# Performance work log

Measured on AMD Instinct MI355X. Metric: run time of the kernel, lower is better.

## Reference

```python
import jax, jax.numpy as jnp
import numpy as np

N_TOKENS = 16384
MODEL_DIM = 2048
NUM_EXPERTS = 16
TOP_K = 2
CAPACITY_FACTOR = 1.0
NUM_SPLIT = 2  # os.environ 'num_split' default in source


def setup_inputs() -> dict:
    key = jax.random.key(0)
    kx, kw = jax.random.split(key)
    x = jax.random.normal(kx, (N_TOKENS, MODEL_DIM), dtype=jnp.float32)
    # kaiming_normal_ on Linear weight: std = sqrt(2 / fan_in)
    wg = jax.random.normal(kw, (NUM_EXPERTS, MODEL_DIM), dtype=jnp.float32) * np.float32(np.sqrt(2.0 / MODEL_DIM))
    return {"x": x, "wg": wg}


def _loss_compute(logits):
    gates = jax.nn.softmax(logits, axis=1)              # [N, E]
    num_experts = logits.shape[1]
    indices1_s = jnp.argmax(gates, axis=1)              # [N]
    mask1 = jax.nn.one_hot(indices1_s, num_experts, dtype=gates.dtype)
    me = jnp.mean(gates, axis=0)
    ce = jnp.mean(mask1, axis=0)
    l_aux = jnp.sum(me * ce) * num_experts
    return l_aux, indices1_s, gates


def _dispatch_fix_capacity(gates, k, capacity_factor, num_split):
    # gates is detached in the original (torch .detach())
    gates = jax.lax.stop_gradient(gates)
    n, e = gates.shape
    capacity = int(k * n // e * capacity_factor) // num_split * num_split
    values, topk_idx = jax.lax.top_k(gates, k)          # [N, k]
    weights = values
    flat_experts = topk_idx.reshape(-1)                 # [N*k]
    order = jnp.argsort(flat_experts)                   # stable sort by expert id
    experts_sorted = flat_experts[order]
    token_ids = jnp.repeat(jnp.arange(n, dtype=jnp.int32), k)[order]
    # position of each routed token within its expert's run
    counts = jax.ops.segment_sum(jnp.ones_like(flat_experts, dtype=jnp.int32), flat_experts, num_segments=e)
    starts = jnp.cumsum(counts) - counts                # exclusive prefix sum
    pos = jnp.arange(n * k, dtype=jnp.int32) - starts[experts_sorted]
    # fixed-capacity index table, -1 = empty slot; overflow tokens dropped
    ind = jnp.full((e, capacity), -1, dtype=jnp.int32)
    ind = ind.at[experts_sorted, pos].set(token_ids, mode="drop")  # pos>=capacity dropped
    indices = ind.reshape(-1)                           # [E*capacity], expert-major
    mask = indices >= 0
    expert_ids = jnp.repeat(jnp.arange(e, dtype=gates.dtype), capacity)
    return weights, indices, expert_ids, mask


def reference(x, wg):
    logits = jnp.einsum("nd,ed->ne", x, wg)             # Linear, no bias
    l_aux, _indices1, gates = _loss_compute(logits)
    weights, indices, expert_ids, mask = _dispatch_fix_capacity(
        gates, TOP_K, CAPACITY_FACTOR, NUM_SPLIT)
    return l_aux, weights, indices, expert_ids
```

## Files before the change

kernel.cpp:

```cpp
#include <hip/hip_runtime.h>
#include <hip/hip_bf16.h>
#include <stdint.h>

#define N_TOKENS    16384
#define MODEL_DIM   2048
#define NUM_EXPERTS 16
#define CAPACITY    2048
#define NBLK2       512
#define NBLK        256
#define GBLK        512
#define W_OFF       1
#define IDX_OFF     (1 + 2 * N_TOKENS)
#define EID_OFF     (IDX_OFF + NUM_EXPERTS * CAPACITY)

#define SC_E01    0
#define SC_CNTH   16384
#define SC_CEH    32768
#define SC_ME     49152

#define DPPX(v, ctrl) __int_as_float(__builtin_amdgcn_update_dpp(             \
    0, __float_as_int(v), (ctrl), 0xF, 0xF, true))
#define SWZ(v, off) __int_as_float(__builtin_amdgcn_ds_swizzle(               \
    __float_as_int(v), (off)))

__global__ __launch_bounds__(512) void k_logits(
    const float* __restrict__ x, const float* __restrict__ wg,
    float* __restrict__ out, uint8_t* __restrict__ ws)
{
  __shared__ float part[8][32][2][17];
  const int tid = threadIdx.x;
  const int b = blockIdx.x;
  const int l = tid & 63;
  const int kr = tid >> 6;
  const int kb = kr * 256 + l * 4;
  const int rot = l & 15;

  float4 w[16];
#pragma unroll
  for (int i = 0; i < NUM_EXPERTS; ++i)
    w[i] = *reinterpret_cast<const float4*>(wg + (size_t)((i ^ rot) * MODEL_DIM) + kb);

  const float* xp = x + (size_t)(b * 32) * MODEL_DIM + kb;
  float4 xva = *reinterpret_cast<const float4*>(xp);
  float4 xvb = *reinterpret_cast<const float4*>(xp + MODEL_DIM);

#pragma unroll 2
  for (int t = 0; t < 32; ++t) {
    float4 xvc;
    if (t < 30)
      xvc = *reinterpret_cast<const float4*>(xp + (size_t)(t + 2) * MODEL_DIM);

    float cur[16];
#pragma unroll
    for (int i = 0; i < NUM_EXPERTS; ++i)
      cur[i] = xva.x * w[i].x + xva.y * w[i].y + xva.z * w[i].z + xva.w * w[i].w;

#pragma unroll
    for (int r = 0; r < 8; ++r) cur[r] = cur[2 * r] + DPPX(cur[2 * r + 1], 0xB1);
#pragma unroll
    for (int r = 0; r < 4; ++r) cur[r] = cur[2 * r] + DPPX(cur[2 * r + 1], 0x4E);
#pragma unroll
    for (int r = 0; r < 2; ++r) cur[r] = cur[2 * r] + SWZ(cur[2 * r + 1], 0x101F);
    float v = cur[0] + DPPX(cur[1], 0x128);
    v += SWZ(v, 0x401F);
    if ((l & 31) < 16) part[kr][t][l >> 5][l & 15] = v;
    xva = xvb; xvb = xvc;
  }
  __syncthreads();

  if (tid < 32) {
    const int tg = b * 32 + tid;
    float logit[NUM_EXPERTS];
#pragma unroll
    for (int e4 = 0; e4 < 4; ++e4) {
      float4 s = *reinterpret_cast<const float4*>(&part[0][tid][0][e4 * 4]);
#pragma unroll
      for (int k2 = 0; k2 < 8; ++k2) {
#pragma unroll
        for (int h = 0; h < 2; ++h) {
          if (k2 == 0 && h == 0) continue;
          float4 p = *reinterpret_cast<const float4*>(&part[k2][tid][h][e4 * 4]);
          s.x += p.x; s.y += p.y; s.z += p.z; s.w += p.w;
        }
      }
      logit[e4 * 4 + 0] = s.x; logit[e4 * 4 + 1] = s.y;
      logit[e4 * 4 + 2] = s.z; logit[e4 * 4 + 3] = s.w;
    }

    float m = logit[0];
#pragma unroll
    for (int e = 1; e < NUM_EXPERTS; e++) m = fmaxf(m, logit[e]);
    float gg[NUM_EXPERTS]; float z = 0.f;
#pragma unroll
    for (int e = 0; e < NUM_EXPERTS; e++) { gg[e] = expf(logit[e] - m); z += gg[e]; }
    float inv = 1.f / z;
#pragma unroll
    for (int e = 0; e < NUM_EXPERTS; e++) gg[e] *= inv;

    float v1 = gg[0], v2 = -1.f; int e1 = 0, e2 = 0;
#pragma unroll
    for (int e = 1; e < NUM_EXPERTS; e++) {
      if (gg[e] > v1) { v2 = v1; e2 = e1; v1 = gg[e]; e1 = e; }
      else if (gg[e] > v2) { v2 = gg[e]; e2 = e; }
    }
    out[W_OFF + 2 * tg]     = v1;
    out[W_OFF + 2 * tg + 1] = v2;
    ws[SC_E01 + tg] = (uint8_t)(e1 | (e2 << 4));

    int mycount = 0, myce = 0;
    for (int e = 0; e < NUM_EXPERTS; e++) {
      unsigned long long m1 = __ballot(e1 == e);
      unsigned long long m2 = __ballot(e2 == e);
      if (tid == e) { mycount = __popcll(m1 | m2); myce = __popcll(m1); }
    }
    if (tid < NUM_EXPERTS) {
      reinterpret_cast<uint16_t*>(ws + SC_CNTH)[tid * NBLK2 + b] = (uint16_t)mycount;
      reinterpret_cast<uint16_t*>(ws + SC_CEH)[tid * NBLK2 + b] = (uint16_t)myce;
    }

#pragma unroll
    for (int e = 0; e < NUM_EXPERTS; e++) {
      gg[e] += __shfl_xor(gg[e], 1, 64);
      gg[e] += __shfl_xor(gg[e], 2, 64);
      gg[e] += __shfl_xor(gg[e], 4, 64);
      gg[e] += __shfl_xor(gg[e], 8, 64);
      gg[e] += __shfl_xor(gg[e], 16, 64);
    }
    if (tid == 0) {
      float* mp = reinterpret_cast<float*>(ws + SC_ME);
#pragma unroll
      for (int e = 0; e < NUM_EXPERTS; e++) mp[b * NUM_EXPERTS + e] = gg[e];
    }
  }
}

__global__ __launch_bounds__(192) void k_tail(
    const uint8_t* __restrict__ ws, float* __restrict__ out) {
  __shared__ int sstart[NUM_EXPERTS];
  __shared__ int stot[NUM_EXPERTS];
  const int tid = threadIdx.x;
  const int b = blockIdx.x;

  if (b == 256) {
    __shared__ float sme2[12][NUM_EXPERTS];
    __shared__ int sce2[12][NUM_EXPERTS];
    const float* me = reinterpret_cast<const float*>(ws + SC_ME);
    const uint16_t* ceh = reinterpret_cast<const uint16_t*>(ws + SC_CEH);
    const int e = tid & 15, grp = tid >> 4;
    float ms = 0.f; int cs = 0;
    for (int k = grp; k < NBLK2; k += 12) {
      ms += me[k * NUM_EXPERTS + e];
      cs += ceh[e * NBLK2 + k];
    }
    sme2[grp][e] = ms; sce2[grp][e] = cs;
    __syncthreads();
    if (tid < NUM_EXPERTS) {
      float ssum = 0.f; int ce = 0;
#pragma unroll
      for (int g2 = 0; g2 < 12; g2++) { ssum += sme2[g2][tid]; ce += sce2[g2][tid]; }
      float prod = (ssum * (1.0f / N_TOKENS)) * ((float)ce * (1.0f / N_TOKENS));
      prod += __shfl_xor(prod, 1, 64);
      prod += __shfl_xor(prod, 2, 64);
      prod += __shfl_xor(prod, 4, 64);
      prod += __shfl_xor(prod, 8, 64);
      if (tid == 0) out[0] = prod * (float)NUM_EXPERTS;
    }
    return;
  }

  if (tid < 64) {
    const int e = tid >> 2, q = tid & 3;
    const uint32_t* row =
        reinterpret_cast<const uint32_t*>(ws + SC_CNTH) + e * (NBLK2 / 2) + q * 64;
    const int limit = 2 * b;
    int s_lt = 0, s_all = 0;
    for (int wd = 0; wd < 64; ++wd) {
      uint32_t v = row[wd];
      int pair = (int)(v & 0xFFFF) + (int)(v >> 16);
      s_all += pair;
      if (q * 128 + 2 * wd < limit) s_lt += pair;
    }
    s_lt += __shfl_xor(s_lt, 1, 64);  s_lt += __shfl_xor(s_lt, 2, 64);
    s_all += __shfl_xor(s_all, 1, 64); s_all += __shfl_xor(s_all, 2, 64);
    if (q == 0) { sstart[e] = s_lt; stot[e] = s_all; }
  }
  __syncthreads();

  if (tid < 64) {
    const int t = b * 64 + tid;
    const int v = ws[SC_E01 + t];
    const int e1 = v & 15, e2 = v >> 4;
    const unsigned long long below = (1ull << tid) - 1ull;
    int p1 = CAPACITY, p2 = CAPACITY;
    for (int e = 0; e < NUM_EXPERTS; e++) {
      unsigned long long m = __ballot(e1 == e) | __ballot(e2 == e);
      int r = __popcll(m & below);
      int sbase = sstart[e];
      if (e1 == e) p1 = sbase + r;
      if (e2 == e) p2 = sbase + r;
    }
    float tf = (float)t;
    if ((unsigned)p1 < (unsigned)CAPACITY) out[IDX_OFF + e1 * CAPACITY + p1] = tf;
    if ((unsigned)p2 < (unsigned)CAPACITY) out[IDX_OFF + e2 * CAPACITY + p2] = tf;
  } else {
    const int slot = b * 128 + (tid - 64);
    const int e = slot >> 11;
    const int p = slot & (CAPACITY - 1);
    if (p >= stot[e]) out[IDX_OFF + slot] = -1.0f;
    out[EID_OFF + slot] = (float)e;
  }
}

extern "C" void kernel_launch(void* const* d_in, const int* in_sizes, int n_in,
                              void* d_out, int out_size, void* d_ws, size_t ws_size,
                              hipStream_t stream) {
  const float* x  = (const float*)d_in[0];
  const float* wg = (const float*)d_in[1];
  float* out = (float*)d_out;
  uint8_t* ws = (uint8_t*)d_ws;

  k_logits<<<GBLK, 512, 0, stream>>>(x, wg, out, ws);
  k_tail<<<257, 192, 0, stream>>>(ws, out);
}
```

Baseline: 48.84 us.

## Split expert dimension across two wave groups with 1024-thread logits blocks

Doubles the logits block to 1024 threads so each half of the waves handles 8 of the 16 experts, halving per-thread weight registers (8 float4 instead of 16) and requesting higher waves per EU. The x prefetch depth drops from two rows to one, and the shared partial-sum layout is reorganized per expert half. This targets latency hiding through higher occupancy, but each x row is now loaded by twice as many waves and there is less prefetch per wave.

Measured after the change: 58.41 us. 19.6% more time.

```diff
diff --git a/kernel.cpp b/kernel.cpp
--- a/kernel.cpp
+++ b/kernel.cpp
@@ -23,48 +23,49 @@
 #define SWZ(v, off) __int_as_float(__builtin_amdgcn_ds_swizzle(               \
     __float_as_int(v), (off)))
 
-__global__ __launch_bounds__(512) void k_logits(
+__global__ void __launch_bounds__(1024)
+__attribute__((amdgpu_waves_per_eu(8))) k_logits(
     const float* __restrict__ x, const float* __restrict__ wg,
     float* __restrict__ out, uint8_t* __restrict__ ws)
 {
-  __shared__ float part[8][32][2][17];
+  __shared__ float part[8][2][2][32][8];
   const int tid = threadIdx.x;
   const int b = blockIdx.x;
   const int l = tid & 63;
-  const int kr = tid >> 6;
+  const int wv = tid >> 6;
+  const int kr = wv & 7;
+  const int eh = wv >> 3;
   const int kb = kr * 256 + l * 4;
-  const int rot = l & 15;
-
-  float4 w[16];
-#pragma unroll
-  for (int i = 0; i < NUM_EXPERTS; ++i)
-    w[i] = *reinterpret_cast<const float4*>(wg + (size_t)((i ^ rot) * MODEL_DIM) + kb);
+  const int rot = l & 7;
+
+  float4 w[8];
+#pragma unroll
+  for (int i = 0; i < 8; ++i)
+    w[i] = *reinterpret_cast<const float4*>(
+        wg + (size_t)((eh * 8 + (i ^ rot)) * MODEL_DIM) + kb);
 
   const float* xp = x + (size_t)(b * 32) * MODEL_DIM + kb;
   float4 xva = *reinterpret_cast<const float4*>(xp);
-  float4 xvb = *reinterpret_cast<const float4*>(xp + MODEL_DIM);
-
-#pragma unroll 2
+
   for (int t = 0; t < 32; ++t) {
-    float4 xvc;
-    if (t < 30)
-      xvc = *reinterpret_cast<const float4*>(xp + (size_t)(t + 2) * MODEL_DIM);
-
-    float cur[16];
-#pragma unroll
-    for (int i = 0; i < NUM_EXPERTS; ++i)
+    float4 xvb;
+    if (t < 31)
+      xvb = *reinterpret_cast<const float4*>(xp + (size_t)(t + 1) * MODEL_DIM);
+
+    float cur[8];
+#pragma unroll
+    for (int i = 0; i < 8; ++i)
       cur[i] = xva.x * w[i].x + xva.y * w[i].y + xva.z * w[i].z + xva.w * w[i].w;
 
 #pragma unroll
-    for (int r = 0; r < 8; ++r) cur[r] = cur[2 * r] + DPPX(cur[2 * r + 1], 0xB1);
-#pragma unroll
-    for (int r = 0; r < 4; ++r) cur[r] = cur[2 * r] + DPPX(cur[2 * r + 1], 0x4E);
-#pragma unroll
-    for (int r = 0; r < 2; ++r) cur[r] = cur[2 * r] + SWZ(cur[2 * r + 1], 0x101F);
-    float v = cur[0] + DPPX(cur[1], 0x128);
+    for (int r = 0; r < 4; ++r) cur[r] = cur[2 * r] + DPPX(cur[2 * r + 1], 0xB1);
+#pragma unroll
+    for (int r = 0; r < 2; ++r) cur[r] = cur[2 * r] + DPPX(cur[2 * r + 1], 0x4E);
+    float v = cur[0] + SWZ(cur[1], 0x101F);
+    v += DPPX(v, 0x128);
     v += SWZ(v, 0x401F);
-    if ((l & 31) < 16) part[kr][t][l >> 5][l & 15] = v;
-    xva = xvb; xvb = xvc;
+    if ((l & 31) < 8) part[kr][eh][l >> 5][t][l & 7] = v;
+    xva = xvb;
   }
   __syncthreads();
 
@@ -73,13 +74,13 @@
     float logit[NUM_EXPERTS];
 #pragma unroll
     for (int e4 = 0; e4 < 4; ++e4) {
-      float4 s = *reinterpret_cast<const float4*>(&part[0][tid][0][e4 * 4]);
+      const int ee = e4 >> 1, oo = (e4 & 1) * 4;
+      float4 s = make_float4(0.f, 0.f, 0.f, 0.f);
 #pragma unroll
       for (int k2 = 0; k2 < 8; ++k2) {
 #pragma unroll
-        for (int h = 0; h < 2; ++h) {
-          if (k2 == 0 && h == 0) continue;
-          float4 p = *reinterpret_cast<const float4*>(&part[k2][tid][h][e4 * 4]);
+        for (int hh = 0; hh < 2; ++hh) {
+          float4 p = *reinterpret_cast<const float4*>(&part[k2][ee][hh][tid][oo]);
           s.x += p.x; s.y += p.y; s.z += p.z; s.w += p.w;
         }
       }
@@ -219,6 +220,6 @@
   float* out = (float*)d_out;
   uint8_t* ws = (uint8_t*)d_ws;
 
-  k_logits<<<GBLK, 512, 0, stream>>>(x, wg, out, ws);
+  k_logits<<<GBLK, 1024, 0, stream>>>(x, wg, out, ws);
   k_tail<<<257, 192, 0, stream>>>(ws, out);
 }
```
